# Performance work log

Measured on AMD Instinct MI355X. Metric: run time of the kernel, lower is better.

## Reference

```python
import jax, jax.numpy as jnp
import numpy as np

# ---- dims (match init_kwargs / input_specs) ----
N = 50000        # nodes
E = 600000       # edges
F_IN = 128       # n_features
HID = 128        # hidden_dims
K = 8            # heads
D_A = 16         # attention dim per head
D_V = 16         # value dim per head
D_M = 64         # max-pool gate dim
CLASSES = 40     # n_classes
LAYERS = 2
SLOPE = 0.1      # negative_slop


def glorot(key, shape):
    lim = jnp.sqrt(6.0 / (shape[-2] + shape[-1]))
    return jax.random.uniform(key, shape, minval=-lim, maxval=lim, dtype=jnp.float32)


def setup_inputs() -> dict:
    key = jax.random.key(0)
    ks = jax.random.split(key, 10)
    x = jax.random.normal(ks[0], (N, F_IN), dtype=jnp.float32)
    edge_index = jax.random.randint(ks[1], (2, E), 0, N, dtype=jnp.int64)
    weight_in = glorot(ks[2], (F_IN, HID))
    weight_out = glorot(ks[3], (HID, CLASSES))
    # per-layer GaANConv params, stacked on leading layer dim
    Wq = glorot(ks[4], (LAYERS, HID, K * D_A))            # query proj
    Wk = glorot(ks[5], (LAYERS, HID, K * D_A))            # key proj
    Wv = glorot(ks[6], (LAYERS, HID, K * D_V))            # value proj
    Wm = glorot(ks[7], (LAYERS, HID, D_M))                # max-pool gate proj
    Wg = glorot(ks[8], (LAYERS, HID + D_M + HID, K))      # gate FC
    Wo = glorot(ks[9], (LAYERS, HID + K * D_V, HID))      # output proj
    return {"x": x, "edge_index": edge_index, "weight_in": weight_in,
            "weight_out": weight_out, "Wq": Wq, "Wk": Wk, "Wv": Wv,
            "Wm": Wm, "Wg": Wg, "Wo": Wo}


def gaan_conv(x, src, dst, wq, wk, wv, wm, wg, wo):
    n = x.shape[0]
    q = (x @ wq).reshape(n, K, D_A)
    k = (x @ wk).reshape(n, K, D_A)
    v = (x @ wv).reshape(n, K, D_V)
    # dot-product attention logits per edge/head: <q_dst, k_src>
    score = jnp.einsum('ekd,ekd->ek', q[dst], k[src])          # [E,K]
    # segment softmax over incoming edges of each dst node
    smax = jax.ops.segment_max(score, dst, num_segments=n)     # [N,K]
    smax = jnp.where(jnp.isfinite(smax), smax, 0.0)            # empty segments -> 0
    ex = jnp.exp(score - smax[dst])
    denom = jax.ops.segment_sum(ex, dst, num_segments=n)
    alpha = ex / (denom[dst] + 1e-16)                          # [E,K]
    agg = jax.ops.segment_sum(alpha[:, :, None] * v[src], dst, num_segments=n)  # [N,K,D_V]
    # gates: sigmoid(FC([x_i, max_j FC_m(x_j), mean_j x_j]))
    m = x @ wm                                                 # [N,D_M]
    maxpool = jax.ops.segment_max(m[src], dst, num_segments=n)
    maxpool = jnp.where(jnp.isfinite(maxpool), maxpool, 0.0)
    deg = jax.ops.segment_sum(jnp.ones((src.shape[0],), x.dtype), dst, num_segments=n)
    meanpool = jax.ops.segment_sum(x[src], dst, num_segments=n) / jnp.maximum(deg, 1.0)[:, None]
    g = jax.nn.sigmoid(jnp.concatenate([x, maxpool, meanpool], axis=1) @ wg)  # [N,K]
    gated = (g[:, :, None] * agg).reshape(n, K * D_V)
    return jnp.concatenate([x, gated], axis=1) @ wo            # [N,HID]


def reference(x, edge_index, weight_in, weight_out, Wq, Wk, Wv, Wm, Wg, Wo):
    src, dst = edge_index[0], edge_index[1]
    h = x @ weight_in
    for i in range(LAYERS):
        h = jax.nn.leaky_relu(
            gaan_conv(h, src, dst, Wq[i], Wk[i], Wv[i], Wm[i], Wg[i], Wo[i]),
            negative_slope=SLOPE)
        # dropout is identity in eval mode
    out = h @ weight_out
    return jax.nn.log_softmax(out, axis=1)
```

## Files before the change

### kernel.cpp

```cpp
#include <hip/hip_runtime.h>
#include <math.h>

#define NNODES 50000
#define NEDGES 600000
#define HIDDIM 128
#define NHEAD 8
#define DM 64
#define NCLS 40
#define FSTR 584
#define OFF_K 128
#define OFF_V 256
#define OFF_M 384
#define OFF_HG 448
#define OFF_H 456
#define NBLK 196

typedef __attribute__((ext_vector_type(8))) short short8;
typedef __attribute__((ext_vector_type(4))) float f32x4;

static __device__ __forceinline__ unsigned short f2bf(float f) {
    unsigned u = __float_as_uint(f);
    unsigned r = (u + 0x7fffu + ((u >> 16) & 1u)) >> 16;
    return (unsigned short)r;
}
static __device__ __forceinline__ float bflo(unsigned u) { return __uint_as_float(u << 16); }
static __device__ __forceinline__ float bfhi(unsigned u) { return __uint_as_float(u & 0xffff0000u); }
static __device__ __forceinline__ float bf2f(unsigned short s) {
    return __uint_as_float(((unsigned)s) << 16);
}

template <int KCHUNKS, int WF32, int WB1, int ACT>
__global__ __launch_bounds__(256) void gemm_1p(
    const unsigned short* __restrict__ A1, int lda1, int K1,
    const unsigned short* __restrict__ A2, int lda2, int K2,
    const unsigned short* __restrict__ BT,
    float* __restrict__ C, int ldc,
    unsigned short* __restrict__ Cb1, int ldb1, int off1,
    int M, int NN)
{
    const int K = KCHUNKS * 32;
    const int l = threadIdx.x & 63, wv = threadIdx.x >> 6;
    const int r = l & 15, g = l >> 4;
    const int row0 = blockIdx.y * 128 + wv * 32;

    short8 a[KCHUNKS][2];
#pragma unroll
    for (int kc = 0; kc < KCHUNKS; ++kc) {
        int kg = kc * 32;
        const unsigned short* Ak;
        int ka, lda;
        if (kg < K1) { Ak = A1; ka = kg; lda = lda1; }
        else         { Ak = A2; ka = kg - K1; lda = lda2; }
#pragma unroll
        for (int m = 0; m < 2; ++m) {
            int row = row0 + m * 16 + r;
            if (row < M)
                a[kc][m] = *reinterpret_cast<const short8*>(Ak + (size_t)row * lda + ka + 8 * g);
            else
                a[kc][m] = short8{0, 0, 0, 0, 0, 0, 0, 0};
        }
    }

    const int ntiles = (NN + 63) >> 6;
    for (int t = 0; t < ntiles; ++t) {
        const int col0 = t * 64;
        f32x4 acc[2][4] = {};
#pragma unroll
        for (int kc = 0; kc < KCHUNKS; ++kc) {
            short8 b[4];
#pragma unroll
            for (int n = 0; n < 4; ++n) {
                int col = col0 + n * 16 + r;
                if (col < NN)
                    b[n] = *reinterpret_cast<const short8*>(BT + (size_t)col * K + kc * 32 + 8 * g);
                else
                    b[n] = short8{0, 0, 0, 0, 0, 0, 0, 0};
            }
#pragma unroll
            for (int m = 0; m < 2; ++m)
#pragma unroll
                for (int n = 0; n < 4; ++n)
                    acc[m][n] = __builtin_amdgcn_mfma_f32_16x16x32_bf16(a[kc][m], b[n], acc[m][n], 0, 0, 0);
        }
#pragma unroll
        for (int m = 0; m < 2; ++m) {
#pragma unroll
            for (int j = 0; j < 4; ++j) {
                int row = row0 + m * 16 + 4 * g + j;
                if (row >= M) continue;
#pragma unroll
                for (int n = 0; n < 4; ++n) {
                    int col = col0 + n * 16 + r;
                    if (col >= NN) continue;
                    float vv = acc[m][n][j];
                    if (ACT) vv = vv > 0.f ? vv : 0.1f * vv;
                    if (WF32) C[(size_t)row * ldc + col] = vv;
                    if (WB1)  Cb1[(size_t)row * ldb1 + off1 + col] = f2bf(vv);
                }
            }
        }
    }
}

#define BT_TOTAL 206848
__global__ __launch_bounds__(256) void pack_weights(
    const float* __restrict__ w_in, const float* __restrict__ w_out,
    const float* __restrict__ Wq, const float* __restrict__ Wk,
    const float* __restrict__ Wv, const float* __restrict__ Wm,
    const float* __restrict__ Wg, const float* __restrict__ Wo,
    unsigned short* __restrict__ BT)
{
    int i = blockIdx.x * 256 + threadIdx.x;
    if (i >= BT_TOTAL) return;
    float val;
    if (i < 16384) {
        int c = i >> 7, k = i & 127;
        val = w_in[k * 128 + c];
    } else if (i < 133120) {
        int li = i - 16384;
        int L = li / 58368, t = li % 58368;
        int c = t >> 7, k = t & 127;
        if      (c < 128) val = Wq[L * 16384 + k * 128 + c];
        else if (c < 256) val = Wk[L * 16384 + k * 128 + (c - 128)];
        else if (c < 384) val = Wv[L * 16384 + k * 128 + (c - 256)];
        else if (c < 448) val = Wm[L * 8192  + k * 64  + (c - 384)];
        else              val = Wg[L * 2560 + (192 + k) * 8 + (c - 448)];
    } else if (i < 198656) {
        int li = i - 133120;
        int L = li / 32768, t = li % 32768;
        int c = t >> 8, k = t & 255;
        val = Wo[L * 32768 + k * 128 + c];
    } else {
        int t = i - 198656;
        int c = t >> 7, k = t & 127;
        val = (c < NCLS) ? w_out[k * NCLS + c] : 0.f;
    }
    BT[i] = f2bf(val);
}

__global__ __launch_bounds__(256) void convert_x_kernel(
    const float* __restrict__ x, unsigned int* __restrict__ xb2)
{
    int i = blockIdx.x * 256 + threadIdx.x;
    if (i >= NNODES * HIDDIM / 2) return;
    float2 f = *reinterpret_cast<const float2*>(x + (size_t)i * 2);
    xb2[i] = (unsigned)f2bf(f.x) | ((unsigned)f2bf(f.y) << 16);
}

__global__ __launch_bounds__(256) void hist_kernel(
    const int* __restrict__ ei, int* __restrict__ degi)
{
    int e = blockIdx.x * 256 + threadIdx.x;
    if (e >= NEDGES) return;
    unsigned d = (unsigned)ei[NEDGES + e]; if (d >= NNODES) d = 0;
    atomicAdd(&degi[d], 1);
}

static __device__ __forceinline__ int wave_incl_scan(int x, int lane) {
#pragma unroll
    for (int off = 1; off < 64; off <<= 1) {
        int n = __shfl_up(x, off);
        if (lane >= off) x += n;
    }
    return x;
}

__global__ __launch_bounds__(256) void scan_blk_kernel(
    const int* __restrict__ degi, int* __restrict__ rowptr,
    int* __restrict__ bsum)
{
    __shared__ int wsum[4];
    const int t = threadIdx.x, b = blockIdx.x;
    const int idx = b * 256 + t;
    const int lane = t & 63, wv = t >> 6;
    int v = (idx < NNODES) ? degi[idx] : 0;
    int incl = wave_incl_scan(v, lane);
    if (lane == 63) wsum[wv] = incl;
    __syncthreads();
    int wpre = 0;
#pragma unroll
    for (int w = 0; w < 4; ++w) wpre += (w < wv) ? wsum[w] : 0;
    if (idx < NNODES) rowptr[idx] = wpre + incl - v;
    if (t == 255) bsum[b] = wpre + incl;
}

__global__ __launch_bounds__(256) void scan_top_kernel(
    const int* __restrict__ bsum, int* __restrict__ boff,
    int* __restrict__ rowptr)
{
    __shared__ int wsum[4];
    const int t = threadIdx.x;
    const int lane = t & 63, wv = t >> 6;
    int v = (t < NBLK) ? bsum[t] : 0;
    int incl = wave_incl_scan(v, lane);
    if (lane == 63) wsum[wv] = incl;
    __syncthreads();
    int wpre = 0;
#pragma unroll
    for (int w = 0; w < 4; ++w) wpre += (w < wv) ? wsum[w] : 0;
    if (t < NBLK) boff[t] = wpre + incl - v;
    if (t == 0) rowptr[NNODES] = NEDGES;
}

__global__ __launch_bounds__(256) void scan_add_kernel(
    int* __restrict__ rowptr, const int* __restrict__ boff)
{
    int idx = blockIdx.x * 256 + threadIdx.x;
    if (idx < NNODES) rowptr[idx] += boff[blockIdx.x];
}

__global__ __launch_bounds__(256) void scatter_kernel(
    const int* __restrict__ ei, const int* __restrict__ rowptr,
    int* __restrict__ fill, int* __restrict__ csr_src)
{
    int e = blockIdx.x * 256 + threadIdx.x;
    if (e >= NEDGES) return;
    unsigned s = (unsigned)ei[e];          if (s >= NNODES) s = 0;
    unsigned d = (unsigned)ei[NEDGES + e]; if (d >= NNODES) d = 0;
    int pos = rowptr[d] + atomicAdd(&fill[d], 1);
    csr_src[pos] = (int)s;
}

__global__ __launch_bounds__(256) void fused_edge_kernel(
    const int* __restrict__ rowptr, const int* __restrict__ csr_src,
    const unsigned short* __restrict__ feat, const float* __restrict__ Wg,
    unsigned short* __restrict__ gatedb)
{
    int node = blockIdx.x * 4 + (threadIdx.x >> 6);
    if (node >= NNODES) return;
    const int lane = threadIdx.x & 63;
    const int c2 = lane * 2;
    const int j0 = lane & 7;

    const int start = rowptr[node], end = rowptr[node + 1];
    const int deg = end - start;

    const unsigned short* frow = feat + (size_t)node * FSTR;
    unsigned qu = *reinterpret_cast<const unsigned*>(frow + c2);
    float qx = bflo(qu), qy = bfhi(qu);

    float mr = -INFINITY, dr = 0.f;
    float a0 = 0.f, a1 = 0.f;
    float hgs = 0.f;
    float mm = -INFINITY;

    int p = start;
    for (; p + 2 <= end; p += 2) {
        int s0 = csr_src[p], s1 = csr_src[p + 1];
        const unsigned short* r0 = feat + (size_t)s0 * FSTR;
        const unsigned short* r1 = feat + (size_t)s1 * FSTR;
        unsigned ku0 = *reinterpret_cast<const unsigned*>(r0 + OFF_K + c2);
        unsigned vu0 = *reinterpret_cast<const unsigned*>(r0 + OFF_V + c2);
        float    mv0 = bf2f(r0[OFF_M + lane]);
        float    hg0 = bf2f(r0[OFF_HG + j0]);
        unsigned ku1 = *reinterpret_cast<const unsigned*>(r1 + OFF_K + c2);
        unsigned vu1 = *reinterpret_cast<const unsigned*>(r1 + OFF_V + c2);
        float    mv1 = bf2f(r1[OFF_M + lane]);
        float    hg1 = bf2f(r1[OFF_HG + j0]);

        float sc0 = qx * bflo(ku0) + qy * bfhi(ku0);
        float sc1 = qx * bflo(ku1) + qy * bfhi(ku1);
        sc0 += __shfl_xor(sc0, 1);  sc1 += __shfl_xor(sc1, 1);
        sc0 += __shfl_xor(sc0, 2);  sc1 += __shfl_xor(sc1, 2);
        sc0 += __shfl_xor(sc0, 4);  sc1 += __shfl_xor(sc1, 4);

        float nm = fmaxf(mr, fmaxf(sc0, sc1));
        float scale = __expf(mr - nm);
        float e0 = __expf(sc0 - nm), e1 = __expf(sc1 - nm);
        dr = dr * scale + e0 + e1;
        a0 = a0 * scale; a0 = fmaf(e0, bflo(vu0), a0); a0 = fmaf(e1, bflo(vu1), a0);
        a1 = a1 * scale; a1 = fmaf(e0, bfhi(vu0), a1); a1 = fmaf(e1, bfhi(vu1), a1);
        mr = nm;

        hgs += hg0 + hg1;
        mm = fmaxf(mm, fmaxf(mv0, mv1));
    }
    if (p < end) {
        int s0 = csr_src[p];
        const unsigned short* r0 = feat + (size_t)s0 * FSTR;
        unsigned ku0 = *reinterpret_cast<const unsigned*>(r0 + OFF_K + c2);
        unsigned vu0 = *reinterpret_cast<const unsigned*>(r0 + OFF_V + c2);
        float    mv0 = bf2f(r0[OFF_M + lane]);
        float    hg0 = bf2f(r0[OFF_HG + j0]);

        float sc0 = qx * bflo(ku0) + qy * bfhi(ku0);
        sc0 += __shfl_xor(sc0, 1);
        sc0 += __shfl_xor(sc0, 2);
        sc0 += __shfl_xor(sc0, 4);

        float nm = fmaxf(mr, sc0);
        float scale = __expf(mr - nm);
        float e0 = __expf(sc0 - nm);
        dr = dr * scale + e0;
        a0 = fmaf(e0, bflo(vu0), a0 * scale);
        a1 = fmaf(e0, bfhi(vu0), a1 * scale);
        mr = nm;

        hgs += hg0;
        mm = fmaxf(mm, mv0);
    }

    float inv  = 1.f / (dr + 1e-16f);
    float invd = 1.f / fmaxf((float)deg, 1.f);
    if (deg == 0) { mm = 0.f; inv = 0.f; }

    unsigned hou = *reinterpret_cast<const unsigned*>(frow + OFF_H + c2);
    float hx = bflo(hou), hy = bfhi(hou);

    const float* w0 = Wg + (size_t)c2 * 8;
    const float* w1 = Wg + (size_t)(c2 + 1) * 8;
    const float* w2 = Wg + (size_t)(128 + lane) * 8;

    float part[8];
#pragma unroll
    for (int j = 0; j < 8; ++j)
        part[j] = hx * w0[j] + hy * w1[j] + mm * w2[j];
#pragma unroll
    for (int off = 1; off < 64; off <<= 1)
#pragma unroll
        for (int j = 0; j < 8; ++j)
            part[j] += __shfl_xor(part[j], off);

    float mc = __shfl(hgs, lane >> 3);
    float gg = 1.f / (1.f + __expf(-(part[lane >> 3] + mc * invd)));
    float o0 = gg * a0 * inv, o1 = gg * a1 * inv;
    unsigned outu = (unsigned)f2bf(o0) | ((unsigned)f2bf(o1) << 16);
    *reinterpret_cast<unsigned*>(gatedb + (size_t)node * HIDDIM + c2) = outu;
}

__global__ __launch_bounds__(256) void logsoftmax_kernel(float* __restrict__ out)
{
    int gt = blockIdx.x * 256 + threadIdx.x;
    int wid = gt >> 6;
    int lane = threadIdx.x & 63;
    if (wid >= NNODES) return;
    float* row = out + (size_t)wid * NCLS;
    float x = (lane < NCLS) ? row[lane] : -INFINITY;
    float mx = x;
#pragma unroll
    for (int off = 32; off; off >>= 1) mx = fmaxf(mx, __shfl_xor(mx, off));
    float ex = (lane < NCLS) ? __expf(x - mx) : 0.f;
    float sm = ex;
#pragma unroll
    for (int off = 32; off; off >>= 1) sm += __shfl_xor(sm, off);
    float lse = mx + logf(sm);
    if (lane < NCLS) row[lane] = x - lse;
}

static inline int cdiv(int a, int b) { return (a + b - 1) / b; }

extern "C" void kernel_launch(void* const* d_in, const int* in_sizes, int n_in,
                              void* d_out, int out_size, void* d_ws, size_t ws_size,
                              hipStream_t stream)
{
    const float* x     = (const float*)d_in[0];
    const int*   ei    = (const int*)d_in[1];
    const float* w_in  = (const float*)d_in[2];
    const float* w_out = (const float*)d_in[3];
    const float* Wq    = (const float*)d_in[4];
    const float* Wk    = (const float*)d_in[5];
    const float* Wv    = (const float*)d_in[6];
    const float* Wm    = (const float*)d_in[7];
    const float* Wg    = (const float*)d_in[8];
    const float* Wo    = (const float*)d_in[9];
    float* out = (float*)d_out;

    const size_t NF = NNODES;
    unsigned short* xb     = (unsigned short*)d_ws;
    unsigned short* feat0  = xb    + NF * 128;
    unsigned short* feat1  = feat0 + NF * FSTR;
    unsigned short* gatedb = feat1 + NF * FSTR;
    unsigned short* BTpool = gatedb + NF * 128;
    int* rowptr  = (int*)(BTpool + BT_TOTAL);
    int* degi    = rowptr + (NNODES + 1);
    int* fill    = degi + NNODES;
    int* csr_src = fill + NNODES;
    int* bsum    = csr_src + NEDGES;
    int* boff    = bsum + NBLK;

    const unsigned short* BTin    = BTpool;
    const unsigned short* BTqkvm0 = BTpool + 16384;
    const unsigned short* BTqkvm1 = BTpool + 74752;
    const unsigned short* BTo0    = BTpool + 133120;
    const unsigned short* BTo1    = BTpool + 165888;
    const unsigned short* BTout   = BTpool + 198656;

    pack_weights<<<cdiv(BT_TOTAL, 256), 256, 0, stream>>>(
        w_in, w_out, Wq, Wk, Wv, Wm, Wg, Wo, BTpool);
    convert_x_kernel<<<cdiv(NNODES * HIDDIM / 2, 256), 256, 0, stream>>>(
        x, (unsigned int*)xb);
    hipMemsetAsync(degi, 0, 2 * NNODES * sizeof(int), stream);
    hist_kernel<<<cdiv(NEDGES, 256), 256, 0, stream>>>(ei, degi);
    scan_blk_kernel<<<NBLK, 256, 0, stream>>>(degi, rowptr, bsum);
    scan_top_kernel<<<1, 256, 0, stream>>>(bsum, boff, rowptr);
    scan_add_kernel<<<NBLK, 256, 0, stream>>>(rowptr, boff);
    scatter_kernel<<<cdiv(NEDGES, 256), 256, 0, stream>>>(ei, rowptr, fill, csr_src);

    const dim3 gM(1, cdiv(NNODES, 128));

    gemm_1p<4, 0, 1, 0><<<gM, 256, 0, stream>>>(
        xb, 128, 128, nullptr, 0, 0, BTin,
        nullptr, 0, feat0, FSTR, OFF_H, NNODES, 128);

    unsigned short* featA = feat0;
    unsigned short* featB = feat1;
    for (int L = 0; L < 2; ++L) {
        const unsigned short* btq = L ? BTqkvm1 : BTqkvm0;
        const unsigned short* bto = L ? BTo1 : BTo0;
        const float* wg = Wg + (size_t)L * 320 * 8;

        gemm_1p<4, 0, 1, 0><<<gM, 256, 0, stream>>>(
            featA + OFF_H, FSTR, 128, nullptr, 0, 0, btq,
            nullptr, 0, featA, FSTR, 0, NNODES, 456);

        fused_edge_kernel<<<cdiv(NNODES, 4), 256, 0, stream>>>(
            rowptr, csr_src, featA, wg, gatedb);

        gemm_1p<8, 0, 1, 1><<<gM, 256, 0, stream>>>(
            featA + OFF_H, FSTR, 128, gatedb, 128, 128, bto,
            nullptr, 0, featB, FSTR, OFF_H, NNODES, 128);

        unsigned short* t = featA; featA = featB; featB = t;
    }

    gemm_1p<4, 1, 0, 0><<<gM, 256, 0, stream>>>(
        featA + OFF_H, FSTR, 128, nullptr, 0, 0, BTout,
        out, NCLS, nullptr, 0, 0, NNODES, NCLS);
    logsoftmax_kernel<<<cdiv(NNODES * 64, 256), 256, 0, stream>>>(out);
}
```

Baseline: 465.4 us.

## Fuse prep kernels, fuse classifier GEMM with log-softmax, shrink GEMM row tiles, lazy softmax rescale

Merges weight packing, x conversion and degree histogram into one prep kernel, removing two launches. The final classifier GEMM now computes log-softmax in registers, so the separate pass over the output is gone. GEMM blocks now cover 64 rows instead of 128, giving more blocks and fewer registers per thread at the cost of reloading B tiles more often. The online softmax in the edge kernel only rescales when the running max rises by more than 8, which skips exp calls but lets terms grow up to e^8 before rescaling.

```diff
diff --git a/kernel.cpp b/kernel.cpp
--- a/kernel.cpp
+++ b/kernel.cpp
@@ -14,6 +14,7 @@
 #define OFF_HG 448
 #define OFF_H 456
 #define NBLK 196
+#define CONV_TOTAL (NNODES * HIDDIM / 2)
 
 typedef __attribute__((ext_vector_type(8))) short short8;
 typedef __attribute__((ext_vector_type(4))) float f32x4;
@@ -29,21 +30,21 @@
     return __uint_as_float(((unsigned)s) << 16);
 }
 
-template <int KCHUNKS, int WF32, int WB1, int ACT>
+template <int KCHUNKS, int ACT>
 __global__ __launch_bounds__(256) void gemm_1p(
     const unsigned short* __restrict__ A1, int lda1, int K1,
     const unsigned short* __restrict__ A2, int lda2, int K2,
     const unsigned short* __restrict__ BT,
-    float* __restrict__ C, int ldc,
     unsigned short* __restrict__ Cb1, int ldb1, int off1,
     int M, int NN)
 {
     const int K = KCHUNKS * 32;
     const int l = threadIdx.x & 63, wv = threadIdx.x >> 6;
     const int r = l & 15, g = l >> 4;
-    const int row0 = blockIdx.y * 128 + wv * 32;
-
-    short8 a[KCHUNKS][2];
+    const int row0 = blockIdx.y * 64 + wv * 16;
+    const int arow = row0 + r;
+
+    short8 a[KCHUNKS];
 #pragma unroll
     for (int kc = 0; kc < KCHUNKS; ++kc) {
         int kg = kc * 32;
@@ -51,20 +52,16 @@
         int ka, lda;
         if (kg < K1) { Ak = A1; ka = kg; lda = lda1; }
         else         { Ak = A2; ka = kg - K1; lda = lda2; }
-#pragma unroll
-        for (int m = 0; m < 2; ++m) {
-            int row = row0 + m * 16 + r;
-            if (row < M)
-                a[kc][m] = *reinterpret_cast<const short8*>(Ak + (size_t)row * lda + ka + 8 * g);
-            else
-                a[kc][m] = short8{0, 0, 0, 0, 0, 0, 0, 0};
-        }
+        if (arow < M)
+            a[kc] = *reinterpret_cast<const short8*>(Ak + (size_t)arow * lda + ka + 8 * g);
+        else
+            a[kc] = short8{0, 0, 0, 0, 0, 0, 0, 0};
     }
 
     const int ntiles = (NN + 63) >> 6;
     for (int t = 0; t < ntiles; ++t) {
         const int col0 = t * 64;
-        f32x4 acc[2][4] = {};
+        f32x4 acc[4] = {};
 #pragma unroll
         for (int kc = 0; kc < KCHUNKS; ++kc) {
             short8 b[4];
@@ -77,83 +74,135 @@
                     b[n] = short8{0, 0, 0, 0, 0, 0, 0, 0};
             }
 #pragma unroll
-            for (int m = 0; m < 2; ++m)
-#pragma unroll
-                for (int n = 0; n < 4; ++n)
-                    acc[m][n] = __builtin_amdgcn_mfma_f32_16x16x32_bf16(a[kc][m], b[n], acc[m][n], 0, 0, 0);
-        }
-#pragma unroll
-        for (int m = 0; m < 2; ++m) {
-#pragma unroll
-            for (int j = 0; j < 4; ++j) {
-                int row = row0 + m * 16 + 4 * g + j;
-                if (row >= M) continue;
-#pragma unroll
-                for (int n = 0; n < 4; ++n) {
-                    int col = col0 + n * 16 + r;
-                    if (col >= NN) continue;
-                    float vv = acc[m][n][j];
-                    if (ACT) vv = vv > 0.f ? vv : 0.1f * vv;
-                    if (WF32) C[(size_t)row * ldc + col] = vv;
-                    if (WB1)  Cb1[(size_t)row * ldb1 + off1 + col] = f2bf(vv);
-                }
+            for (int n = 0; n < 4; ++n)
+                acc[n] = __builtin_amdgcn_mfma_f32_16x16x32_bf16(a[kc], b[n], acc[n], 0, 0, 0);
+        }
+#pragma unroll
+        for (int j = 0; j < 4; ++j) {
+            int row = row0 + 4 * g + j;
+            if (row >= M) continue;
+#pragma unroll
+            for (int n = 0; n < 4; ++n) {
+                int col = col0 + n * 16 + r;
+                if (col >= NN) continue;
+                float vv = acc[n][j];
+                if (ACT) vv = vv > 0.f ? vv : 0.1f * vv;
+                Cb1[(size_t)row * ldb1 + off1 + col] = f2bf(vv);
             }
         }
     }
 }
 
+__global__ __launch_bounds__(256) void gemm_cls_lsm(
+    const unsigned short* __restrict__ A, int lda,
+    const unsigned short* __restrict__ BT,
+    float* __restrict__ out, int M)
+{
+    const int l = threadIdx.x & 63, wv = threadIdx.x >> 6;
+    const int r = l & 15, g = l >> 4;
+    const int row0 = blockIdx.y * 64 + wv * 16;
+    const int arow = row0 + r;
+
+    short8 a[4];
+#pragma unroll
+    for (int kc = 0; kc < 4; ++kc) {
+        if (arow < M)
+            a[kc] = *reinterpret_cast<const short8*>(A + (size_t)arow * lda + kc * 32 + 8 * g);
+        else
+            a[kc] = short8{0, 0, 0, 0, 0, 0, 0, 0};
+    }
+    f32x4 acc[4] = {};
+#pragma unroll
+    for (int kc = 0; kc < 4; ++kc) {
+        short8 b[4];
+#pragma unroll
+        for (int n = 0; n < 4; ++n) {
+            int col = n * 16 + r;
+            b[n] = *reinterpret_cast<const short8*>(BT + (size_t)col * 128 + kc * 32 + 8 * g);
+        }
+#pragma unroll
+        for (int n = 0; n < 4; ++n)
+            acc[n] = __builtin_amdgcn_mfma_f32_16x16x32_bf16(a[kc], b[n], acc[n], 0, 0, 0);
+    }
+#pragma unroll
+    for (int j = 0; j < 4; ++j) {
+        int row = row0 + 4 * g + j;
+        float mx = -INFINITY;
+#pragma unroll
+        for (int n = 0; n < 4; ++n) {
+            int col = n * 16 + r;
+            if (col < NCLS) mx = fmaxf(mx, acc[n][j]);
+        }
+        mx = fmaxf(mx, __shfl_xor(mx, 1));
+        mx = fmaxf(mx, __shfl_xor(mx, 2));
+        mx = fmaxf(mx, __shfl_xor(mx, 4));
+        mx = fmaxf(mx, __shfl_xor(mx, 8));
+        float sm = 0.f;
+#pragma unroll
+        for (int n = 0; n < 4; ++n) {
+            int col = n * 16 + r;
+            if (col < NCLS) sm += __expf(acc[n][j] - mx);
+        }
+        sm += __shfl_xor(sm, 1);
+        sm += __shfl_xor(sm, 2);
+        sm += __shfl_xor(sm, 4);
+        sm += __shfl_xor(sm, 8);
+        float lse = mx + logf(sm);
+        if (row < M) {
+#pragma unroll
+            for (int n = 0; n < 4; ++n) {
+                int col = n * 16 + r;
+                if (col < NCLS) out[(size_t)row * NCLS + col] = acc[n][j] - lse;
+            }
+        }
+    }
+}
+
 #define BT_TOTAL 206848
-__global__ __launch_bounds__(256) void pack_weights(
+__global__ __launch_bounds__(256) void prep_kernel(
+    const float* __restrict__ x, const int* __restrict__ ei,
     const float* __restrict__ w_in, const float* __restrict__ w_out,
     const float* __restrict__ Wq, const float* __restrict__ Wk,
     const float* __restrict__ Wv, const float* __restrict__ Wm,
     const float* __restrict__ Wg, const float* __restrict__ Wo,
-    unsigned short* __restrict__ BT)
+    unsigned short* __restrict__ BT, unsigned int* __restrict__ xb2,
+    int* __restrict__ degi)
 {
     int i = blockIdx.x * 256 + threadIdx.x;
-    if (i >= BT_TOTAL) return;
-    float val;
-    if (i < 16384) {
-        int c = i >> 7, k = i & 127;
-        val = w_in[k * 128 + c];
-    } else if (i < 133120) {
-        int li = i - 16384;
-        int L = li / 58368, t = li % 58368;
-        int c = t >> 7, k = t & 127;
-        if      (c < 128) val = Wq[L * 16384 + k * 128 + c];
-        else if (c < 256) val = Wk[L * 16384 + k * 128 + (c - 128)];
-        else if (c < 384) val = Wv[L * 16384 + k * 128 + (c - 256)];
-        else if (c < 448) val = Wm[L * 8192  + k * 64  + (c - 384)];
-        else              val = Wg[L * 2560 + (192 + k) * 8 + (c - 448)];
-    } else if (i < 198656) {
-        int li = i - 133120;
-        int L = li / 32768, t = li % 32768;
-        int c = t >> 8, k = t & 255;
-        val = Wo[L * 32768 + k * 128 + c];
-    } else {
-        int t = i - 198656;
-        int c = t >> 7, k = t & 127;
-        val = (c < NCLS) ? w_out[k * NCLS + c] : 0.f;
-    }
-    BT[i] = f2bf(val);
-}
-
-__global__ __launch_bounds__(256) void convert_x_kernel(
-    const float* __restrict__ x, unsigned int* __restrict__ xb2)
-{
-    int i = blockIdx.x * 256 + threadIdx.x;
-    if (i >= NNODES * HIDDIM / 2) return;
-    float2 f = *reinterpret_cast<const float2*>(x + (size_t)i * 2);
-    xb2[i] = (unsigned)f2bf(f.x) | ((unsigned)f2bf(f.y) << 16);
-}
-
-__global__ __launch_bounds__(256) void hist_kernel(
-    const int* __restrict__ ei, int* __restrict__ degi)
-{
-    int e = blockIdx.x * 256 + threadIdx.x;
-    if (e >= NEDGES) return;
-    unsigned d = (unsigned)ei[NEDGES + e]; if (d >= NNODES) d = 0;
-    atomicAdd(&degi[d], 1);
+    if (i < CONV_TOTAL) {
+        float2 f = *reinterpret_cast<const float2*>(x + (size_t)i * 2);
+        xb2[i] = (unsigned)f2bf(f.x) | ((unsigned)f2bf(f.y) << 16);
+    }
+    if (i < NEDGES) {
+        unsigned d = (unsigned)ei[NEDGES + i]; if (d >= NNODES) d = 0;
+        atomicAdd(&degi[d], 1);
+    }
+    if (i < BT_TOTAL) {
+        float val;
+        if (i < 16384) {
+            int c = i >> 7, k = i & 127;
+            val = w_in[k * 128 + c];
+        } else if (i < 133120) {
+            int li = i - 16384;
+            int L = li / 58368, t = li % 58368;
+            int c = t >> 7, k = t & 127;
+            if      (c < 128) val = Wq[L * 16384 + k * 128 + c];
+            else if (c < 256) val = Wk[L * 16384 + k * 128 + (c - 128)];
+            else if (c < 384) val = Wv[L * 16384 + k * 128 + (c - 256)];
+            else if (c < 448) val = Wm[L * 8192  + k * 64  + (c - 384)];
+            else              val = Wg[L * 2560 + (192 + k) * 8 + (c - 448)];
+        } else if (i < 198656) {
+            int li = i - 133120;
+            int L = li / 32768, t = li % 32768;
+            int c = t >> 8, k = t & 255;
+            val = Wo[L * 32768 + k * 128 + c];
+        } else {
+            int t = i - 198656;
+            int c = t >> 7, k = t & 127;
+            val = (c < NCLS) ? w_out[k * NCLS + c] : 0.f;
+        }
+        BT[i] = f2bf(val);
+    }
 }
 
 static __device__ __forceinline__ int wave_incl_scan(int x, int lane) {
@@ -264,13 +313,16 @@
         sc0 += __shfl_xor(sc0, 2);  sc1 += __shfl_xor(sc1, 2);
         sc0 += __shfl_xor(sc0, 4);  sc1 += __shfl_xor(sc1, 4);
 
-        float nm = fmaxf(mr, fmaxf(sc0, sc1));
-        float scale = __expf(mr - nm);
-        float e0 = __expf(sc0 - nm), e1 = __expf(sc1 - nm);
-        dr = dr * scale + e0 + e1;
-        a0 = a0 * scale; a0 = fmaf(e0, bflo(vu0), a0); a0 = fmaf(e1, bflo(vu1), a0);
-        a1 = a1 * scale; a1 = fmaf(e0, bfhi(vu0), a1); a1 = fmaf(e1, bfhi(vu1), a1);
-        mr = nm;
+        float pm = fmaxf(sc0, sc1);
+        if (pm > mr + 8.f) {
+            float scale = __expf(mr - pm);
+            dr *= scale; a0 *= scale; a1 *= scale;
+            mr = pm;
+        }
+        float e0 = __expf(sc0 - mr), e1 = __expf(sc1 - mr);
+        dr += e0 + e1;
+        a0 = fmaf(e0, bflo(vu0), a0); a0 = fmaf(e1, bflo(vu1), a0);
+        a1 = fmaf(e0, bfhi(vu0), a1); a1 = fmaf(e1, bfhi(vu1), a1);
 
         hgs += hg0 + hg1;
         mm = fmaxf(mm, fmaxf(mv0, mv1));
@@ -288,13 +340,15 @@
         sc0 += __shfl_xor(sc0, 2);
         sc0 += __shfl_xor(sc0, 4);
 
-        float nm = fmaxf(mr, sc0);
-        float scale = __expf(mr - nm);
-        float e0 = __expf(sc0 - nm);
-        dr = dr * scale + e0;
-        a0 = fmaf(e0, bflo(vu0), a0 * scale);
-        a1 = fmaf(e0, bfhi(vu0), a1 * scale);
-        mr = nm;
+        if (sc0 > mr + 8.f) {
+            float scale = __expf(mr - sc0);
+            dr *= scale; a0 *= scale; a1 *= scale;
+            mr = sc0;
+        }
+        float e0 = __expf(sc0 - mr);
+        dr += e0;
+        a0 = fmaf(e0, bflo(vu0), a0);
+        a1 = fmaf(e0, bfhi(vu0), a1);
 
         hgs += hg0;
         mm = fmaxf(mm, mv0);
@@ -326,25 +380,6 @@
     float o0 = gg * a0 * inv, o1 = gg * a1 * inv;
     unsigned outu = (unsigned)f2bf(o0) | ((unsigned)f2bf(o1) << 16);
     *reinterpret_cast<unsigned*>(gatedb + (size_t)node * HIDDIM + c2) = outu;
-}
-
-__global__ __launch_bounds__(256) void logsoftmax_kernel(float* __restrict__ out)
-{
-    int gt = blockIdx.x * 256 + threadIdx.x;
-    int wid = gt >> 6;
-    int lane = threadIdx.x & 63;
-    if (wid >= NNODES) return;
-    float* row = out + (size_t)wid * NCLS;
-    float x = (lane < NCLS) ? row[lane] : -INFINITY;
-    float mx = x;
-#pragma unroll
-    for (int off = 32; off; off >>= 1) mx = fmaxf(mx, __shfl_xor(mx, off));
-    float ex = (lane < NCLS) ? __expf(x - mx) : 0.f;
-    float sm = ex;
-#pragma unroll
-    for (int off = 32; off; off >>= 1) sm += __shfl_xor(sm, off);
-    float lse = mx + logf(sm);
-    if (lane < NCLS) row[lane] = x - lse;
 }
 
 static inline int cdiv(int a, int b) { return (a + b - 1) / b; }
@@ -385,22 +420,20 @@
     const unsigned short* BTo1    = BTpool + 165888;
     const unsigned short* BTout   = BTpool + 198656;
 
-    pack_weights<<<cdiv(BT_TOTAL, 256), 256, 0, stream>>>(
-        w_in, w_out, Wq, Wk, Wv, Wm, Wg, Wo, BTpool);
-    convert_x_kernel<<<cdiv(NNODES * HIDDIM / 2, 256), 256, 0, stream>>>(
-        x, (unsigned int*)xb);
     hipMemsetAsync(degi, 0, 2 * NNODES * sizeof(int), stream);
-    hist_kernel<<<cdiv(NEDGES, 256), 256, 0, stream>>>(ei, degi);
+    prep_kernel<<<cdiv(CONV_TOTAL, 256), 256, 0, stream>>>(
+        x, ei, w_in, w_out, Wq, Wk, Wv, Wm, Wg, Wo,
+        BTpool, (unsigned int*)xb, degi);
     scan_blk_kernel<<<NBLK, 256, 0, stream>>>(degi, rowptr, bsum);
     scan_top_kernel<<<1, 256, 0, stream>>>(bsum, boff, rowptr);
     scan_add_kernel<<<NBLK, 256, 0, stream>>>(rowptr, boff);
     scatter_kernel<<<cdiv(NEDGES, 256), 256, 0, stream>>>(ei, rowptr, fill, csr_src);
 
-    const dim3 gM(1, cdiv(NNODES, 128));
-
-    gemm_1p<4, 0, 1, 0><<<gM, 256, 0, stream>>>(
+    const dim3 gM(1, cdiv(NNODES, 64));
+
+    gemm_1p<4, 0><<<gM, 256, 0, stream>>>(
         xb, 128, 128, nullptr, 0, 0, BTin,
-        nullptr, 0, feat0, FSTR, OFF_H, NNODES, 128);
+        feat0, FSTR, OFF_H, NNODES, 128);
 
     unsigned short* featA = feat0;
     unsigned short* featB = feat1;
@@ -409,22 +442,20 @@
         const unsigned short* bto = L ? BTo1 : BTo0;
         const float* wg = Wg + (size_t)L * 320 * 8;
 
-        gemm_1p<4, 0, 1, 0><<<gM, 256, 0, stream>>>(
+        gemm_1p<4, 0><<<gM, 256, 0, stream>>>(
             featA + OFF_H, FSTR, 128, nullptr, 0, 0, btq,
-            nullptr, 0, featA, FSTR, 0, NNODES, 456);
+            featA, FSTR, 0, NNODES, 456);
 
         fused_edge_kernel<<<cdiv(NNODES, 4), 256, 0, stream>>>(
             rowptr, csr_src, featA, wg, gatedb);
 
-        gemm_1p<8, 0, 1, 1><<<gM, 256, 0, stream>>>(
+        gemm_1p<8, 1><<<gM, 256, 0, stream>>>(
             featA + OFF_H, FSTR, 128, gatedb, 128, 128, bto,
-            nullptr, 0, featB, FSTR, OFF_H, NNODES, 128);
+            featB, FSTR, OFF_H, NNODES, 128);
 
         unsigned short* t = featA; featA = featB; featB = t;
     }
 
-    gemm_1p<4, 1, 0, 0><<<gM, 256, 0, stream>>>(
-        featA + OFF_H, FSTR, 128, nullptr, 0, 0, BTout,
-        out, NCLS, nullptr, 0, 0, NNODES, NCLS);
-    logsoftmax_kernel<<<cdiv(NNODES * 64, 256), 256, 0, stream>>>(out);
-}
+    gemm_cls_lsm<<<gM, 256, 0, stream>>>(
+        featA + OFF_H, FSTR, BTout, out, NNODES);
+}
```

After: 528.6 us. +13.6%, slower.
